# Kernel optimization log

Hardware: AMD Instinct MI355X
Metric: run time of the kernel (lower is better)

## Reference

```python
import jax, jax.numpy as jnp
import numpy as np

B, S, H = 2, 2048, 2048
N_HEADS, N_KV, HEAD_DIM = 16, 8, 128
EPS = 1e-6
ROPE_THETA = 1e6


def _rms_norm(x, w, eps=EPS):
    # per-head RMSNorm over last dim (head_dim), computed in fp32
    xf = x.astype(jnp.float32)
    var = jnp.mean(xf * xf, axis=-1, keepdims=True)
    return (w * (xf * jax.lax.rsqrt(var + eps))).astype(x.dtype)


def _rotate_half(x):
    x1, x2 = jnp.split(x, 2, axis=-1)
    return jnp.concatenate((-x2, x1), axis=-1)


def setup_inputs() -> dict:
    key = jax.random.key(0)
    ks = jax.random.split(key, 6)
    hidden_states = jax.random.normal(ks[0], (B, S, H), dtype=jnp.float32)
    # RoPE tables: [B, S, head_dim]
    inv_freq = 1.0 / (ROPE_THETA ** (np.arange(0, HEAD_DIM, 2, dtype=np.float32) / HEAD_DIM))
    pos = np.arange(S, dtype=np.float32)
    freqs = np.outer(pos, inv_freq)                      # [S, head_dim/2]
    emb = np.concatenate([freqs, freqs], axis=-1)        # [S, head_dim]
    cos = jnp.broadcast_to(jnp.asarray(np.cos(emb)), (B, S, HEAD_DIM))
    sin = jnp.broadcast_to(jnp.asarray(np.sin(emb)), (B, S, HEAD_DIM))
    # additive causal mask [B, 1, S, S]
    causal = jnp.triu(jnp.full((S, S), -1e9, dtype=jnp.float32), k=1)
    attention_mask = jnp.broadcast_to(causal[None, None], (B, 1, S, S))
    scale = 0.02
    Wq = jax.random.normal(ks[1], (N_HEADS * HEAD_DIM, H), dtype=jnp.float32) * scale
    Wk = jax.random.normal(ks[2], (N_KV * HEAD_DIM, H), dtype=jnp.float32) * scale
    Wv = jax.random.normal(ks[3], (N_KV * HEAD_DIM, H), dtype=jnp.float32) * scale
    Wo = jax.random.normal(ks[4], (H, N_HEADS * HEAD_DIM), dtype=jnp.float32) * scale
    q_norm_w = jnp.ones((HEAD_DIM,), dtype=jnp.float32)
    k_norm_w = jnp.ones((HEAD_DIM,), dtype=jnp.float32)
    return dict(hidden_states=hidden_states, cos=cos, sin=sin,
                attention_mask=attention_mask, Wq=Wq, Wk=Wk, Wv=Wv, Wo=Wo,
                q_norm_w=q_norm_w, k_norm_w=k_norm_w)


def reference(hidden_states, cos, sin, attention_mask, Wq, Wk, Wv, Wo, q_norm_w, k_norm_w):
    b, s, _ = hidden_states.shape
    scaling = HEAD_DIM ** -0.5
    n_rep = N_HEADS // N_KV
    # QKV projections (torch Linear: x @ W.T), split into heads
    q = jnp.einsum('bsh,dh->bsd', hidden_states, Wq).reshape(b, s, N_HEADS, HEAD_DIM)
    k = jnp.einsum('bsh,dh->bsd', hidden_states, Wk).reshape(b, s, N_KV, HEAD_DIM)
    v = jnp.einsum('bsh,dh->bsd', hidden_states, Wv).reshape(b, s, N_KV, HEAD_DIM)
    # per-head QK RMSNorm, then [B, H, S, D]
    q = _rms_norm(q, q_norm_w).transpose(0, 2, 1, 3)
    k = _rms_norm(k, k_norm_w).transpose(0, 2, 1, 3)
    v = v.transpose(0, 2, 1, 3)
    # RoPE (cos/sin unsqueezed over head dim)
    c = cos[:, None, :, :]
    sn = sin[:, None, :, :]
    q = q * c + _rotate_half(q) * sn
    k = k * c + _rotate_half(k) * sn
    # GQA: repeat kv heads
    k = jnp.repeat(k, n_rep, axis=1)
    v = jnp.repeat(v, n_rep, axis=1)
    # eager attention: materialize full [B, H, S, S] scores
    attn_weights = jnp.einsum('bhqd,bhkd->bhqk', q, k) * scaling + attention_mask
    attn_weights = jax.nn.softmax(attn_weights.astype(jnp.float32), axis=-1).astype(q.dtype)
    attn_output = jnp.einsum('bhqk,bhkd->bhqd', attn_weights, v)
    attn_output = attn_output.transpose(0, 2, 1, 3).reshape(b, s, N_HEADS * HEAD_DIM)
    attn_output = jnp.einsum('bsd,hd->bsh', attn_output, Wo)
    return attn_output, attn_weights
```

## Files before the change

### kernel.cpp

```cpp
#include <hip/hip_runtime.h>
#include <stdint.h>

typedef unsigned short u16;
typedef __attribute__((ext_vector_type(8))) short bf16x8;
typedef __attribute__((ext_vector_type(4))) float f32x4;
typedef __attribute__((ext_vector_type(8))) unsigned short u16x8;

#define SCALE_LOG2E 0.12751743007633614f

__device__ __forceinline__ u16 f2bf(float x){
  uint32_t u = __float_as_uint(x);
  u += 0x7FFFu + ((u >> 16) & 1u);
  return (u16)(u >> 16);
}
__device__ __forceinline__ float bf2f(u16 h){
  return __uint_as_float(((uint32_t)h) << 16);
}
__device__ __forceinline__ void gload16(const void* g, void* l){
  __builtin_amdgcn_global_load_lds((const __attribute__((address_space(1))) void*)g,
                                   (__attribute__((address_space(3))) void*)l, 16, 0, 0);
}

__global__ __launch_bounds__(256) void k_cvt5(
    const float* __restrict__ s0, u16* __restrict__ d0,
    const float* __restrict__ s1, u16* __restrict__ d1,
    const float* __restrict__ s2, u16* __restrict__ d2,
    const float* __restrict__ s3, u16* __restrict__ d3,
    const float* __restrict__ s4, u16* __restrict__ d4)
{
  int b = blockIdx.x;
  const float* s; u16* d; int off;
  if      (b < 8192)  { s=s0; d=d0; off=b; }
  else if (b < 12288) { s=s1; d=d1; off=b-8192; }
  else if (b < 14336) { s=s2; d=d2; off=b-12288; }
  else if (b < 16384) { s=s3; d=d3; off=b-14336; }
  else                { s=s4; d=d4; off=b-16384; }
  size_t i = ((size_t)off * 256 + threadIdx.x) * 4;
  float4 v = *(const float4*)(s + i);
  ushort4 o;
  o.x = f2bf(v.x); o.y = f2bf(v.y); o.z = f2bf(v.z); o.w = f2bf(v.w);
  *(ushort4*)(d + i) = o;
}

#define STAGE_UNIT(PTR, ROWOFF, BUF, TENS, KS, T1) do{ \
  _Pragma("unroll") \
  for(int jj=0;jj<2;jj++){ \
    int rs_ = wid*32 + jj*16 + (lane>>2); \
    int kp_ = (lane&3) ^ ((rs_>>1)&3); \
    gload16((PTR) + (size_t)((ROWOFF)+rs_)*K + (size_t)(T1)*64 + (KS)*32 + kp_*8, \
            &lds[BUF][TENS][KS][(wid*2+jj)*512]); \
  }}while(0)

#define FRAG(BASE, ROW) (*(const bf16x8*)((BASE) + (ROW)*32 + ((c_ ^ (((ROW)>>1)&3))<<3)))

__global__ __launch_bounds__(512,2) void k_gemm256(
    const u16* __restrict__ A, const u16* __restrict__ Bw, void* __restrict__ Cout,
    int N, int K, int ldc, int out_f32)
{
  __shared__ u16 lds[2][2][2][256*32];
  const int tid = threadIdx.x, wid = tid>>6, lane = tid&63;
  const int nbn = N >> 8;
  const int cpx = gridDim.x >> 3;
  const int bid = (blockIdx.x & 7)*cpx + (blockIdx.x >> 3);
  const int bm = bid / nbn, bn = bid % nbn;
  const int m0 = bm<<8, n0 = bn<<8;
  const int wm = wid>>2, wn = wid&3;
  const int c_ = lane>>4, rl = lane&15;

  f32x4 acc[8][4];
  f32x4 zero4 = {0.f,0.f,0.f,0.f};
#pragma unroll
  for (int i=0;i<8;i++)
#pragma unroll
    for (int j=0;j<4;j++) acc[i][j] = zero4;

  STAGE_UNIT(A,  m0, 0, 0, 0, 0);
  STAGE_UNIT(Bw, n0, 0, 1, 0, 0);
  STAGE_UNIT(A,  m0, 0, 0, 1, 0);
  STAGE_UNIT(Bw, n0, 0, 1, 1, 0);

  const int nt = K >> 6;
#pragma unroll 2
  for (int t=0; t<nt; ++t) {
    const int cur = t&1, nxt = cur^1;
    const bool pf = (t+1 < nt);
    const u16* Ab0 = lds[cur][0][0];
    const u16* Bb0 = lds[cur][1][0];
    const u16* Ab1 = lds[cur][0][1];
    const u16* Bb1 = lds[cur][1][1];
    bf16x8 af[4], bf[4];

    asm volatile("s_waitcnt vmcnt(4)" ::: "memory");
    __builtin_amdgcn_s_barrier();
    asm volatile("" ::: "memory");
#pragma unroll
    for (int j=0;j<4;j++) bf[j] = FRAG(Bb0, wn*64 + j*16 + rl);
#pragma unroll
    for (int i=0;i<4;i++) af[i] = FRAG(Ab0, wm*128 + i*16 + rl);
    if (pf) STAGE_UNIT(A, m0, nxt, 0, 0, t+1);
    __builtin_amdgcn_s_setprio(1);
#pragma unroll
    for (int i=0;i<4;i++)
#pragma unroll
      for (int j=0;j<4;j++)
        acc[i][j] = __builtin_amdgcn_mfma_f32_16x16x32_bf16(af[i], bf[j], acc[i][j], 0,0,0);
    __builtin_amdgcn_s_setprio(0);
    __builtin_amdgcn_s_barrier();
    asm volatile("" ::: "memory");

#pragma unroll
    for (int i=0;i<4;i++) af[i] = FRAG(Ab0, wm*128 + (i+4)*16 + rl);
    if (pf) STAGE_UNIT(Bw, n0, nxt, 1, 0, t+1);
    __builtin_amdgcn_s_setprio(1);
#pragma unroll
    for (int i=0;i<4;i++)
#pragma unroll
      for (int j=0;j<4;j++)
        acc[i+4][j] = __builtin_amdgcn_mfma_f32_16x16x32_bf16(af[i], bf[j], acc[i+4][j], 0,0,0);
    __builtin_amdgcn_s_setprio(0);
    __builtin_amdgcn_s_barrier();
    asm volatile("" ::: "memory");

    if (pf) { asm volatile("s_waitcnt vmcnt(4)" ::: "memory"); }
    else    { asm volatile("s_waitcnt vmcnt(0)" ::: "memory"); }
    __builtin_amdgcn_s_barrier();
    asm volatile("" ::: "memory");
#pragma unroll
    for (int j=0;j<4;j++) bf[j] = FRAG(Bb1, wn*64 + j*16 + rl);
#pragma unroll
    for (int i=0;i<4;i++) af[i] = FRAG(Ab1, wm*128 + i*16 + rl);
    if (pf) STAGE_UNIT(A, m0, nxt, 0, 1, t+1);
    __builtin_amdgcn_s_setprio(1);
#pragma unroll
    for (int i=0;i<4;i++)
#pragma unroll
      for (int j=0;j<4;j++)
        acc[i][j] = __builtin_amdgcn_mfma_f32_16x16x32_bf16(af[i], bf[j], acc[i][j], 0,0,0);
    __builtin_amdgcn_s_setprio(0);
    __builtin_amdgcn_s_barrier();
    asm volatile("" ::: "memory");

#pragma unroll
    for (int i=0;i<4;i++) af[i] = FRAG(Ab1, wm*128 + (i+4)*16 + rl);
    if (pf) STAGE_UNIT(Bw, n0, nxt, 1, 1, t+1);
    __builtin_amdgcn_s_setprio(1);
#pragma unroll
    for (int i=0;i<4;i++)
#pragma unroll
      for (int j=0;j<4;j++)
        acc[i+4][j] = __builtin_amdgcn_mfma_f32_16x16x32_bf16(af[i], bf[j], acc[i+4][j], 0,0,0);
    __builtin_amdgcn_s_setprio(0);
    __builtin_amdgcn_s_barrier();
    asm volatile("" ::: "memory");
  }

  const int r0 = m0 + wm*128 + ((lane>>4)<<2);
  const int c0 = n0 + wn*64 + rl;
  if (out_f32) {
    float* C = (float*)Cout;
#pragma unroll
    for (int i=0;i<8;i++)
#pragma unroll
      for (int j=0;j<4;j++)
#pragma unroll
        for (int r=0;r<4;r++)
          C[(size_t)(r0 + i*16 + r)*ldc + (c0 + j*16)] = acc[i][j][r];
  } else {
    u16* C = (u16*)Cout;
#pragma unroll
    for (int i=0;i<8;i++)
#pragma unroll
      for (int j=0;j<4;j++)
#pragma unroll
        for (int r=0;r<4;r++)
          C[(size_t)(r0 + i*16 + r)*ldc + (c0 + j*16)] = f2bf(acc[i][j][r]);
  }
}

#define STAGE_A128(BUF, KS, T1) do{ \
  int rs_ = wid*16 + (lane>>2); \
  int kp_ = (lane&3) ^ ((rs_>>1)&3); \
  gload16(A + (size_t)(m0+rs_)*K + (size_t)(T1)*64 + (KS)*32 + kp_*8, \
          &ldsA[BUF][KS][wid*512]); \
  }while(0)

#define STAGE_B128(BUF, KS, T1) do{ \
  _Pragma("unroll") \
  for(int jj=0;jj<2;jj++){ \
    int rs_ = wid*32 + jj*16 + (lane>>2); \
    int kp_ = (lane&3) ^ ((rs_>>1)&3); \
    gload16(Bw + (size_t)(n0+rs_)*K + (size_t)(T1)*64 + (KS)*32 + kp_*8, \
            &ldsB[BUF][KS][(wid*2+jj)*512]); \
  }}while(0)

__global__ __launch_bounds__(512,2) void k_gemm_bm128(
    const u16* __restrict__ A, const u16* __restrict__ Bw, float* __restrict__ C,
    int N, int K, int ldc)
{
  __shared__ u16 ldsA[2][2][128*32];
  __shared__ u16 ldsB[2][2][256*32];
  const int tid = threadIdx.x, wid = tid>>6, lane = tid&63;
  const int nbn = N >> 8;
  const int cpx = gridDim.x >> 3;
  const int bid = (blockIdx.x & 7)*cpx + (blockIdx.x >> 3);
  const int bm = bid / nbn, bn = bid % nbn;
  const int m0 = bm<<7, n0 = bn<<8;
  const int wm = wid>>2, wn = wid&3;
  const int c_ = lane>>4, rl = lane&15;

  f32x4 acc[4][4];
  f32x4 zero4 = {0.f,0.f,0.f,0.f};
#pragma unroll
  for (int i=0;i<4;i++)
#pragma unroll
    for (int j=0;j<4;j++) acc[i][j] = zero4;

  STAGE_A128(0, 0, 0);
  STAGE_B128(0, 0, 0);
  STAGE_A128(0, 1, 0);
  STAGE_B128(0, 1, 0);

  const int nt = K >> 6;
#pragma unroll 2
  for (int t=0; t<nt; ++t) {
    const int cur = t&1, nxt = cur^1;
    const bool pf = (t+1 < nt);
    bf16x8 af[4], bf[4];

    asm volatile("s_waitcnt vmcnt(3)" ::: "memory");
    __builtin_amdgcn_s_barrier();
    asm volatile("" ::: "memory");
#pragma unroll
    for (int i=0;i<4;i++) af[i] = FRAG(ldsA[cur][0], wm*64 + i*16 + rl);
#pragma unroll
    for (int j=0;j<4;j++) bf[j] = FRAG(ldsB[cur][0], wn*64 + j*16 + rl);
    if (pf) { STAGE_A128(nxt, 0, t+1); STAGE_B128(nxt, 0, t+1); }
    __builtin_amdgcn_s_setprio(1);
#pragma unroll
    for (int i=0;i<4;i++)
#pragma unroll
      for (int j=0;j<4;j++)
        acc[i][j] = __builtin_amdgcn_mfma_f32_16x16x32_bf16(af[i], bf[j], acc[i][j], 0,0,0);
    __builtin_amdgcn_s_setprio(0);
    __builtin_amdgcn_s_barrier();
    asm volatile("" ::: "memory");

    if (pf) { asm volatile("s_waitcnt vmcnt(3)" ::: "memory"); }
    else    { asm volatile("s_waitcnt vmcnt(0)" ::: "memory"); }
    __builtin_amdgcn_s_barrier();
    asm volatile("" ::: "memory");
#pragma unroll
    for (int i=0;i<4;i++) af[i] = FRAG(ldsA[cur][1], wm*64 + i*16 + rl);
#pragma unroll
    for (int j=0;j<4;j++) bf[j] = FRAG(ldsB[cur][1], wn*64 + j*16 + rl);
    if (pf) { STAGE_A128(nxt, 1, t+1); STAGE_B128(nxt, 1, t+1); }
    __builtin_amdgcn_s_setprio(1);
#pragma unroll
    for (int i=0;i<4;i++)
#pragma unroll
      for (int j=0;j<4;j++)
        acc[i][j] = __builtin_amdgcn_mfma_f32_16x16x32_bf16(af[i], bf[j], acc[i][j], 0,0,0);
    __builtin_amdgcn_s_setprio(0);
    __builtin_amdgcn_s_barrier();
    asm volatile("" ::: "memory");
  }

  const int r0 = m0 + wm*64 + ((lane>>4)<<2);
  const int c0 = n0 + wn*64 + rl;
#pragma unroll
  for (int i=0;i<4;i++)
#pragma unroll
    for (int j=0;j<4;j++)
#pragma unroll
      for (int r=0;r<4;r++)
        C[(size_t)(r0 + i*16 + r)*ldc + (c0 + j*16)] = acc[i][j][r];
}

__global__ __launch_bounds__(256) void k_normrope(
    u16* __restrict__ qkv, const float* __restrict__ cosb, const float* __restrict__ sinb,
    const float* __restrict__ qw, const float* __restrict__ kw)
{
  const int tid = threadIdx.x, lane = tid&63;
  const int task = blockIdx.x*4 + (tid>>6);
  int bs, col; const float* w;
  if (task < 65536) { bs = task >> 4; col = (task & 15)*128; w = qw; }
  else { int t2 = task - 65536; bs = t2 >> 3; col = 2048 + (t2 & 7)*128; w = kw; }
  u16* row = qkv + (size_t)bs*4096 + col;
  float x0 = bf2f(row[lane]), x1 = bf2f(row[lane+64]);
  float ss = x0*x0 + x1*x1;
#pragma unroll
  for (int m=1; m<64; m<<=1) ss += __shfl_xor(ss, m, 64);
  float rn = rsqrtf(ss*(1.0f/128.0f) + 1e-6f);
  const float* cp = cosb + (size_t)bs*128;
  const float* sp = sinb + (size_t)bs*128;
  float q0 = x0*rn*w[lane], q1 = x1*rn*w[lane+64];
  float o0 = q0*cp[lane]    - q1*sp[lane];
  float o1 = q1*cp[lane+64] + q0*sp[lane+64];
  row[lane]    = f2bf(o0);
  row[lane+64] = f2bf(o1);
}

__global__ __launch_bounds__(256) void k_vtrans(const u16* __restrict__ qkv, u16* __restrict__ vt)
{
  const int bid = blockIdx.x;
  const int dt = bid & 1, st = (bid>>1)&31, kvh = (bid>>6)&7, b = bid>>9;
  __shared__ u16 tile[64][72];
  const int tid = threadIdx.x;
  const int rr = tid >> 3, c = (tid & 7) * 8;
  const u16* src = qkv + ((size_t)(b*2048 + st*64))*4096 + 3072 + kvh*128 + dt*64;
#pragma unroll
  for (int p=0;p<2;p++){
    int sl = p*32 + rr;
    u16x8 v = *(const u16x8*)(src + (size_t)sl*4096 + c);
#pragma unroll
    for (int e=0;e<8;e++) tile[sl][c+e] = v[e];
  }
  __syncthreads();
  u16* dst = vt + ((size_t)((b*8+kvh)*128 + dt*64))*2048 + st*64;
#pragma unroll
  for (int p=0;p<2;p++){
    int dl = p*32 + rr;
    u16x8 o;
#pragma unroll
    for (int e=0;e<8;e++) o[e] = tile[c+e][dl];
    *(u16x8*)(dst + (size_t)dl*2048 + c) = o;
  }
}

#define STAGE_K(T, DSTBUF) do { \
  _Pragma("unroll") \
  for (int i_=0;i_<4;i_++){ \
    int r_ = wv*16 + i_*4 + (lane>>4); \
    int cs_ = (lane&15) ^ (r_&7); \
    gload16(Kb + (size_t)((T)*64 + r_)*4096 + cs_*8, (DSTBUF) + (wv*4+i_)*512); \
  } } while(0)

#define STAGE_V(T, DSTBUF) do { \
  _Pragma("unroll") \
  for (int i_=0;i_<4;i_++){ \
    int d_ = wv*32 + i_*8 + (lane>>3); \
    int cs_ = (lane&7) ^ (d_&7); \
    gload16(Vb + (size_t)d_*2048 + (T)*64 + cs_*8, (DSTBUF) + (wv*4+i_)*512); \
  } } while(0)

#define COMPUTE_S(SACC, KBUF) do { \
  _Pragma("unroll") \
  for (int ks_=0;ks_<4;ks_++){ \
    bf16x8 bfr_[4]; \
    _Pragma("unroll") \
    for (int ns_=0;ns_<4;ns_++){ \
      int n_ = ns_*16 + (lane&15); \
      int sl_ = (ks_*4 + (lane>>4)) ^ (n_&7); \
      bfr_[ns_] = *(const bf16x8*)((KBUF) + n_*128 + sl_*8); \
    } \
    _Pragma("unroll") \
    for (int ms_=0;ms_<2;ms_++) \
      _Pragma("unroll") \
      for (int ns_=0;ns_<4;ns_++) \
        SACC[ms_][ns_] = __builtin_amdgcn_mfma_f32_16x16x32_bf16(qf[ms_][ks_], bfr_[ns_], SACC[ms_][ns_], 0,0,0); \
  } } while(0)

__global__ __launch_bounds__(256) void k_attn(
    const u16* __restrict__ qkv, const u16* __restrict__ vt,
    float* __restrict__ probs, u16* __restrict__ attn_o)
{
  __shared__ u16 lK[2][64*128];
  __shared__ u16 lV[2][128*64];
  __shared__ u16 lP[4][32*64];
  const int tid = threadIdx.x, wv = tid>>6, lane = tid&63;
  const int bid = blockIdx.x;
  const int r9 = bid >> 5;
  const int qt = (r9 < 8) ? (15 - r9) : (r9 - 8);
  const int bh = bid & 31;
  const int h = bh & 15, b = bh >> 4;
  const int kvh = h>>1;
  const int q0 = qt<<7;
  const u16* Qb = qkv + (size_t)b*2048*4096 + h*128;
  const u16* Kb = qkv + (size_t)b*2048*4096 + 2048 + kvh*128;
  const u16* Vb = vt + (size_t)(b*8+kvh)*128*2048;

  f32x4 zero4 = {0.f,0.f,0.f,0.f};

  bf16x8 qf[2][4];
#pragma unroll
  for (int ms=0;ms<2;ms++)
#pragma unroll
    for (int ks=0;ks<4;ks++){
      int r = q0 + wv*32 + ms*16 + (lane&15);
      int cc = ks*32 + (lane>>4)*8;
      qf[ms][ks] = *(const bf16x8*)(Qb + (size_t)r*4096 + cc);
    }

  const int nkt = 2*qt + 2;
  float lsum[2][4];
#pragma unroll
  for (int ms=0;ms<2;ms++)
#pragma unroll
    for (int r=0;r<4;r++) lsum[ms][r] = 0.f;

  int cur = 0;
  STAGE_K(0, lK[0]);
  asm volatile("s_waitcnt vmcnt(0)" ::: "memory");
  __syncthreads();
  for (int t=0; t<nkt; ++t) {
    if (t+1 < nkt) STAGE_K(t+1, lK[cur^1]);
    f32x4 sacc[2][4];
#pragma unroll
    for (int ms=0;ms<2;ms++)
#pragma unroll
      for (int ns=0;ns<4;ns++) sacc[ms][ns] = zero4;
    COMPUTE_S(sacc, lK[cur]);
    const int rb = q0 + wv*32 + ((lane>>4)<<2);
    const int cb = t*64 + (lane&15);
#pragma unroll
    for (int ms=0;ms<2;ms++)
#pragma unroll
      for (int ns=0;ns<4;ns++)
#pragma unroll
        for (int r=0;r<4;r++){
          int rg = rb + ms*16 + r, cg = cb + ns*16;
          float e = __builtin_exp2f(sacc[ms][ns][r]*SCALE_LOG2E);
          lsum[ms][r] += (cg <= rg) ? e : 0.f;
        }
    asm volatile("s_waitcnt vmcnt(0)" ::: "memory");
    __syncthreads();
    cur ^= 1;
  }
#pragma unroll
  for (int m=1;m<16;m<<=1)
#pragma unroll
    for (int ms=0;ms<2;ms++)
#pragma unroll
      for (int r=0;r<4;r++) lsum[ms][r] += __shfl_xor(lsum[ms][r], m, 64);
  float linv[2][4];
#pragma unroll
  for (int ms=0;ms<2;ms++)
#pragma unroll
    for (int r=0;r<4;r++) linv[ms][r] = 1.0f / lsum[ms][r];

  f32x4 oacc[2][8];
#pragma unroll
  for (int ms=0;ms<2;ms++)
#pragma unroll
    for (int nd=0;nd<8;nd++) oacc[ms][nd] = zero4;

  u16* pw = lP[wv];
  float* pb = probs + (size_t)(b*16+h)*2048*2048;

  cur = 0;
  STAGE_K(0, lK[0]);
  STAGE_V(0, lV[0]);
  asm volatile("s_waitcnt vmcnt(0)" ::: "memory");
  __syncthreads();
  for (int t=0; t<nkt; ++t) {
    if (t+1 < nkt) { STAGE_K(t+1, lK[cur^1]); STAGE_V(t+1, lV[cur^1]); }
    asm volatile("" ::: "memory");
    f32x4 sacc[2][4];
#pragma unroll
    for (int ms=0;ms<2;ms++)
#pragma unroll
      for (int ns=0;ns<4;ns++) sacc[ms][ns] = zero4;
    COMPUTE_S(sacc, lK[cur]);
    const int rb = q0 + wv*32 + ((lane>>4)<<2);
    const int cb = t*64 + (lane&15);
#pragma unroll
    for (int ms=0;ms<2;ms++)
#pragma unroll
      for (int ns=0;ns<4;ns++)
#pragma unroll
        for (int r=0;r<4;r++){
          int rg = rb + ms*16 + r, cg = cb + ns*16;
          float p = (cg <= rg) ? __builtin_exp2f(sacc[ms][ns][r]*SCALE_LOG2E)*linv[ms][r] : 0.f;
          __builtin_nontemporal_store(p, pb + (size_t)rg*2048 + cg);
          int ql = ms*16 + ((lane>>4)<<2) + r;
          int kl = ns*16 + (lane&15);
          pw[ql*64 + (((kl>>3) ^ (ql&7))<<3) + (kl&7)] = f2bf(p);
        }
    const u16* vbuf = lV[cur];
#pragma unroll
    for (int kks=0;kks<2;kks++){
      bf16x8 pa[2];
#pragma unroll
      for (int ms=0;ms<2;ms++){
        int ql = ms*16 + (lane&15);
        int sl = (kks*4 + (lane>>4)) ^ (ql&7);
        pa[ms] = *(const bf16x8*)(pw + ql*64 + sl*8);
      }
#pragma unroll
      for (int nd=0;nd<8;nd++){
        int d = nd*16 + (lane&15);
        int sl = (kks*4 + (lane>>4)) ^ (d&7);
        bf16x8 vb = *(const bf16x8*)(vbuf + d*64 + sl*8);
#pragma unroll
        for (int ms=0;ms<2;ms++)
          oacc[ms][nd] = __builtin_amdgcn_mfma_f32_16x16x32_bf16(pa[ms], vb, oacc[ms][nd], 0,0,0);
      }
    }
    if (t+1 < nkt) {
      asm volatile("s_waitcnt vmcnt(32)" ::: "memory");
      __syncthreads();
    }
    cur ^= 1;
  }

  const int kend = nkt*64;
  f32x4 z4 = {0.f,0.f,0.f,0.f};
  for (int q = wv*32; q < wv*32+32; ++q){
    float* rp = pb + (size_t)(q0 + q)*2048;
    for (int c = kend + lane*4; c < 2048; c += 256)
      __builtin_nontemporal_store(z4, (f32x4*)(rp + c));
  }

#pragma unroll
  for (int ms=0;ms<2;ms++)
#pragma unroll
    for (int nd=0;nd<8;nd++)
#pragma unroll
      for (int r=0;r<4;r++){
        int rg = q0 + wv*32 + ms*16 + ((lane>>4)<<2) + r;
        int cg = h*128 + nd*16 + (lane&15);
        attn_o[(size_t)(b*2048 + rg)*2048 + cg] = f2bf(oacc[ms][nd][r]);
      }
}

extern "C" void kernel_launch(void* const* d_in, const int* in_sizes, int n_in,
                              void* d_out, int out_size, void* d_ws, size_t ws_size,
                              hipStream_t stream) {
  (void)in_sizes; (void)n_in; (void)out_size; (void)ws_size;
  const float* hs   = (const float*)d_in[0];
  const float* cosb = (const float*)d_in[1];
  const float* sinb = (const float*)d_in[2];
  const float* Wq   = (const float*)d_in[4];
  const float* Wk   = (const float*)d_in[5];
  const float* Wv   = (const float*)d_in[6];
  const float* Wo   = (const float*)d_in[7];
  const float* qw   = (const float*)d_in[8];
  const float* kw   = (const float*)d_in[9];
  float* out   = (float*)d_out;
  float* probs = out + 8388608;

  char* ws = (char*)d_ws;
  u16* hs_b   = (u16*)(ws);
  u16* attn_o = hs_b;
  u16* W_all  = (u16*)(ws + (16u<<20));
  u16* Wo_b   = (u16*)(ws + (32u<<20));
  u16* qkv    = (u16*)(ws + (40u<<20));
  u16* v_t    = (u16*)(ws + (72u<<20));

  k_cvt5<<<20480,256,0,stream>>>(hs, hs_b, Wq, W_all, Wk, W_all + 4194304,
                                 Wv, W_all + 6291456, Wo, Wo_b);

  k_gemm256<<<256,512,0,stream>>>(hs_b, W_all, (void*)qkv, 4096, 2048, 4096, 0);
  k_normrope<<<24576,256,0,stream>>>(qkv, cosb, sinb, qw, kw);
  k_vtrans<<<1024,256,0,stream>>>(qkv, v_t);
  k_attn<<<512,256,0,stream>>>(qkv, v_t, probs, attn_o);
  k_gemm_bm128<<<256,512,0,stream>>>(attn_o, Wo_b, out, 2048, 2048, 2048);
}
```

Baseline: 376.0 us.

## Deepen K prefetch, skip masked tiles per wave, vectorize probability stores

Reworks the attention kernel in several ways. The pass that computes row sums now uses a 4-buffer K ring with prefetch three tiles ahead. Each wave skips score tiles past its own causal diagonal, and the mask test is applied only on the diagonal tile. In the output pass, probabilities are read back from the bf16 LDS tile and written as 16-byte float4 nontemporal stores instead of scalar stores. The trailing zero-fill then starts at each wave's diagonal. The stored fp32 probabilities now hold bf16-rounded values, which loses some precision, and waitcnt counts are hand-tuned.

```diff
diff --git a/kernel.cpp b/kernel.cpp
--- a/kernel.cpp
+++ b/kernel.cpp
@@ -4,6 +4,7 @@
 typedef unsigned short u16;
 typedef __attribute__((ext_vector_type(8))) short bf16x8;
 typedef __attribute__((ext_vector_type(4))) float f32x4;
+typedef __attribute__((ext_vector_type(4))) unsigned short u16x4;
 typedef __attribute__((ext_vector_type(8))) unsigned short u16x8;
 
 #define SCALE_LOG2E 0.12751743007633614f
@@ -364,8 +365,7 @@
     const u16* __restrict__ qkv, const u16* __restrict__ vt,
     float* __restrict__ probs, u16* __restrict__ attn_o)
 {
-  __shared__ u16 lK[2][64*128];
-  __shared__ u16 lV[2][128*64];
+  __shared__ u16 lKV[4][64*128];
   __shared__ u16 lP[4][32*64];
   const int tid = threadIdx.x, wv = tid>>6, lane = tid&63;
   const int bid = blockIdx.x;
@@ -392,118 +392,148 @@
     }
 
   const int nkt = 2*qt + 2;
+  const int tdiag = 2*qt + (wv>>1);
   float lsum[2][4];
 #pragma unroll
   for (int ms=0;ms<2;ms++)
 #pragma unroll
     for (int r=0;r<4;r++) lsum[ms][r] = 0.f;
 
+  STAGE_K(0, lKV[0]);
+  STAGE_K(1, lKV[1]);
+  if (nkt > 2) STAGE_K(2, lKV[2]);
+  for (int t=0; t<nkt; ++t) {
+    if      (t+2 < nkt) { asm volatile("s_waitcnt vmcnt(8)" ::: "memory"); }
+    else if (t+1 < nkt) { asm volatile("s_waitcnt vmcnt(4)" ::: "memory"); }
+    else                { asm volatile("s_waitcnt vmcnt(0)" ::: "memory"); }
+    __syncthreads();
+    if (t+3 < nkt) STAGE_K(t+3, lKV[(t+3)&3]);
+    asm volatile("" ::: "memory");
+    if (t <= tdiag) {
+      f32x4 sacc[2][4];
+#pragma unroll
+      for (int ms=0;ms<2;ms++)
+#pragma unroll
+        for (int ns=0;ns<4;ns++) sacc[ms][ns] = zero4;
+      COMPUTE_S(sacc, lKV[t&3]);
+      const int rb = q0 + wv*32 + ((lane>>4)<<2);
+      const int cb = t*64 + (lane&15);
+      if (t == tdiag) {
+#pragma unroll
+        for (int ms=0;ms<2;ms++)
+#pragma unroll
+          for (int ns=0;ns<4;ns++)
+#pragma unroll
+            for (int r=0;r<4;r++){
+              int rg = rb + ms*16 + r, cg = cb + ns*16;
+              float e = __builtin_exp2f(sacc[ms][ns][r]*SCALE_LOG2E);
+              lsum[ms][r] += (cg <= rg) ? e : 0.f;
+            }
+      } else {
+#pragma unroll
+        for (int ms=0;ms<2;ms++)
+#pragma unroll
+          for (int ns=0;ns<4;ns++)
+#pragma unroll
+            for (int r=0;r<4;r++)
+              lsum[ms][r] += __builtin_exp2f(sacc[ms][ns][r]*SCALE_LOG2E);
+      }
+    }
+  }
+#pragma unroll
+  for (int m=1;m<16;m<<=1)
+#pragma unroll
+    for (int ms=0;ms<2;ms++)
+#pragma unroll
+      for (int r=0;r<4;r++) lsum[ms][r] += __shfl_xor(lsum[ms][r], m, 64);
+  float linv[2][4];
+#pragma unroll
+  for (int ms=0;ms<2;ms++)
+#pragma unroll
+    for (int r=0;r<4;r++) linv[ms][r] = 1.0f / lsum[ms][r];
+
+  f32x4 oacc[2][8];
+#pragma unroll
+  for (int ms=0;ms<2;ms++)
+#pragma unroll
+    for (int nd=0;nd<8;nd++) oacc[ms][nd] = zero4;
+
+  u16* pw = lP[wv];
+  float* pb = probs + (size_t)(b*16+h)*2048*2048;
+
   int cur = 0;
-  STAGE_K(0, lK[0]);
+  STAGE_K(0, lKV[0]);
+  STAGE_V(0, lKV[2]);
   asm volatile("s_waitcnt vmcnt(0)" ::: "memory");
   __syncthreads();
   for (int t=0; t<nkt; ++t) {
-    if (t+1 < nkt) STAGE_K(t+1, lK[cur^1]);
-    f32x4 sacc[2][4];
-#pragma unroll
-    for (int ms=0;ms<2;ms++)
-#pragma unroll
-      for (int ns=0;ns<4;ns++) sacc[ms][ns] = zero4;
-    COMPUTE_S(sacc, lK[cur]);
-    const int rb = q0 + wv*32 + ((lane>>4)<<2);
-    const int cb = t*64 + (lane&15);
-#pragma unroll
-    for (int ms=0;ms<2;ms++)
-#pragma unroll
-      for (int ns=0;ns<4;ns++)
-#pragma unroll
-        for (int r=0;r<4;r++){
-          int rg = rb + ms*16 + r, cg = cb + ns*16;
-          float e = __builtin_exp2f(sacc[ms][ns][r]*SCALE_LOG2E);
-          lsum[ms][r] += (cg <= rg) ? e : 0.f;
+    const bool pf = (t+1 < nkt);
+    if (pf) { STAGE_K(t+1, lKV[cur^1]); STAGE_V(t+1, lKV[2+(cur^1)]); }
+    asm volatile("" ::: "memory");
+    if (t <= tdiag) {
+      f32x4 sacc[2][4];
+#pragma unroll
+      for (int ms=0;ms<2;ms++)
+#pragma unroll
+        for (int ns=0;ns<4;ns++) sacc[ms][ns] = zero4;
+      COMPUTE_S(sacc, lKV[cur]);
+      const int rb = q0 + wv*32 + ((lane>>4)<<2);
+      const int cb = t*64 + (lane&15);
+#pragma unroll
+      for (int ms=0;ms<2;ms++)
+#pragma unroll
+        for (int ns=0;ns<4;ns++)
+#pragma unroll
+          for (int r=0;r<4;r++){
+            int rg = rb + ms*16 + r, cg = cb + ns*16;
+            float p = (cg <= rg) ? __builtin_exp2f(sacc[ms][ns][r]*SCALE_LOG2E)*linv[ms][r] : 0.f;
+            int ql = ms*16 + ((lane>>4)<<2) + r;
+            int kl = ns*16 + (lane&15);
+            pw[ql*64 + (((kl>>3) ^ (ql&7))<<3) + (kl&7)] = f2bf(p);
+          }
+      {
+        const int cq = lane&15, grp = cq>>1, off = (cq&1)*4;
+#pragma unroll
+        for (int it=0; it<8; ++it){
+          int row = it*4 + (lane>>4);
+          int slot = grp ^ (row&7);
+          u16x4 pk4 = *(const u16x4*)(pw + row*64 + slot*8 + off);
+          f32x4 pf4;
+#pragma unroll
+          for (int r=0;r<4;r++) pf4[r] = bf2f(pk4[r]);
+          __builtin_nontemporal_store(pf4,
+            (f32x4*)(pb + (size_t)(q0 + wv*32 + row)*2048 + t*64 + cq*4));
         }
-    asm volatile("s_waitcnt vmcnt(0)" ::: "memory");
-    __syncthreads();
-    cur ^= 1;
-  }
-#pragma unroll
-  for (int m=1;m<16;m<<=1)
-#pragma unroll
-    for (int ms=0;ms<2;ms++)
-#pragma unroll
-      for (int r=0;r<4;r++) lsum[ms][r] += __shfl_xor(lsum[ms][r], m, 64);
-  float linv[2][4];
-#pragma unroll
-  for (int ms=0;ms<2;ms++)
-#pragma unroll
-    for (int r=0;r<4;r++) linv[ms][r] = 1.0f / lsum[ms][r];
-
-  f32x4 oacc[2][8];
-#pragma unroll
-  for (int ms=0;ms<2;ms++)
-#pragma unroll
-    for (int nd=0;nd<8;nd++) oacc[ms][nd] = zero4;
-
-  u16* pw = lP[wv];
-  float* pb = probs + (size_t)(b*16+h)*2048*2048;
-
-  cur = 0;
-  STAGE_K(0, lK[0]);
-  STAGE_V(0, lV[0]);
-  asm volatile("s_waitcnt vmcnt(0)" ::: "memory");
-  __syncthreads();
-  for (int t=0; t<nkt; ++t) {
-    if (t+1 < nkt) { STAGE_K(t+1, lK[cur^1]); STAGE_V(t+1, lV[cur^1]); }
-    asm volatile("" ::: "memory");
-    f32x4 sacc[2][4];
-#pragma unroll
-    for (int ms=0;ms<2;ms++)
-#pragma unroll
-      for (int ns=0;ns<4;ns++) sacc[ms][ns] = zero4;
-    COMPUTE_S(sacc, lK[cur]);
-    const int rb = q0 + wv*32 + ((lane>>4)<<2);
-    const int cb = t*64 + (lane&15);
-#pragma unroll
-    for (int ms=0;ms<2;ms++)
-#pragma unroll
-      for (int ns=0;ns<4;ns++)
-#pragma unroll
-        for (int r=0;r<4;r++){
-          int rg = rb + ms*16 + r, cg = cb + ns*16;
-          float p = (cg <= rg) ? __builtin_exp2f(sacc[ms][ns][r]*SCALE_LOG2E)*linv[ms][r] : 0.f;
-          __builtin_nontemporal_store(p, pb + (size_t)rg*2048 + cg);
-          int ql = ms*16 + ((lane>>4)<<2) + r;
-          int kl = ns*16 + (lane&15);
-          pw[ql*64 + (((kl>>3) ^ (ql&7))<<3) + (kl&7)] = f2bf(p);
+      }
+      const u16* vbuf = lKV[2+cur];
+#pragma unroll
+      for (int kks=0;kks<2;kks++){
+        bf16x8 pa[2];
+#pragma unroll
+        for (int ms=0;ms<2;ms++){
+          int ql = ms*16 + (lane&15);
+          int sl = (kks*4 + (lane>>4)) ^ (ql&7);
+          pa[ms] = *(const bf16x8*)(pw + ql*64 + sl*8);
         }
-    const u16* vbuf = lV[cur];
-#pragma unroll
-    for (int kks=0;kks<2;kks++){
-      bf16x8 pa[2];
-#pragma unroll
-      for (int ms=0;ms<2;ms++){
-        int ql = ms*16 + (lane&15);
-        int sl = (kks*4 + (lane>>4)) ^ (ql&7);
-        pa[ms] = *(const bf16x8*)(pw + ql*64 + sl*8);
-      }
-#pragma unroll
-      for (int nd=0;nd<8;nd++){
-        int d = nd*16 + (lane&15);
-        int sl = (kks*4 + (lane>>4)) ^ (d&7);
-        bf16x8 vb = *(const bf16x8*)(vbuf + d*64 + sl*8);
-#pragma unroll
-        for (int ms=0;ms<2;ms++)
-          oacc[ms][nd] = __builtin_amdgcn_mfma_f32_16x16x32_bf16(pa[ms], vb, oacc[ms][nd], 0,0,0);
+#pragma unroll
+        for (int nd=0;nd<8;nd++){
+          int d = nd*16 + (lane&15);
+          int sl = (kks*4 + (lane>>4)) ^ (d&7);
+          bf16x8 vb = *(const bf16x8*)(vbuf + d*64 + sl*8);
+#pragma unroll
+          for (int ms=0;ms<2;ms++)
+            oacc[ms][nd] = __builtin_amdgcn_mfma_f32_16x16x32_bf16(pa[ms], vb, oacc[ms][nd], 0,0,0);
+        }
       }
     }
-    if (t+1 < nkt) {
-      asm volatile("s_waitcnt vmcnt(32)" ::: "memory");
+    if (pf) {
+      asm volatile("s_waitcnt vmcnt(8)" ::: "memory");
       __syncthreads();
     }
     cur ^= 1;
   }
 
-  const int kend = nkt*64;
+  const int kend = (tdiag+1)*64;
   f32x4 z4 = {0.f,0.f,0.f,0.f};
   for (int q = wv*32; q < wv*32+32; ++q){
     float* rp = pb + (size_t)(q0 + q)*2048;
```

Measured after the change: 358.9 us. 1.05x faster.

## Split softmax row-sum into separate tile-parallel kernel and shrink attention q-tile

Applied to the files above, without the earlier changes.

Moves the first pass (softmax denominators) into its own kernel. That kernel spreads the causal lower-triangle 64x64 tiles evenly across blocks and accumulates row sums with atomics. The main attention kernel now uses 64-row q tiles, giving 1024 blocks, and reads the precomputed sums. It writes probabilities as coalesced float4 stores from the bf16 LDS tile instead of scattered scalar stores. This trades extra Q/K reloads, atomics and a memset for better load balance, higher occupancy and better store coalescing. The stored probabilities are now bf16-rounded values.

```diff
diff --git a/kernel.cpp b/kernel.cpp
--- a/kernel.cpp
+++ b/kernel.cpp
@@ -4,6 +4,7 @@
 typedef unsigned short u16;
 typedef __attribute__((ext_vector_type(8))) short bf16x8;
 typedef __attribute__((ext_vector_type(4))) float f32x4;
+typedef __attribute__((ext_vector_type(4))) unsigned short u16x4;
 typedef __attribute__((ext_vector_type(8))) unsigned short u16x8;
 
 #define SCALE_LOG2E 0.12751743007633614f
@@ -343,7 +344,7 @@
     gload16(Vb + (size_t)d_*2048 + (T)*64 + cs_*8, (DSTBUF) + (wv*4+i_)*512); \
   } } while(0)
 
-#define COMPUTE_S(SACC, KBUF) do { \
+#define COMPUTE_S16(SACC, KBUF) do { \
   _Pragma("unroll") \
   for (int ks_=0;ks_<4;ks_++){ \
     bf16x8 bfr_[4]; \
@@ -354,173 +355,214 @@
       bfr_[ns_] = *(const bf16x8*)((KBUF) + n_*128 + sl_*8); \
     } \
     _Pragma("unroll") \
-    for (int ms_=0;ms_<2;ms_++) \
-      _Pragma("unroll") \
-      for (int ns_=0;ns_<4;ns_++) \
-        SACC[ms_][ns_] = __builtin_amdgcn_mfma_f32_16x16x32_bf16(qf[ms_][ks_], bfr_[ns_], SACC[ms_][ns_], 0,0,0); \
+    for (int ns_=0;ns_<4;ns_++) \
+      SACC[ns_] = __builtin_amdgcn_mfma_f32_16x16x32_bf16(qf[ks_], bfr_[ns_], SACC[ns_], 0,0,0); \
   } } while(0)
 
-__global__ __launch_bounds__(256) void k_attn(
+__global__ __launch_bounds__(256) void k_lsum(
+    const u16* __restrict__ qkv, float* __restrict__ lsum)
+{
+  __shared__ u16 lK[2][64*128];
+  const int tid = threadIdx.x, wv = tid>>6, lane = tid&63;
+  const int rl = lane&15, hi = lane>>4;
+  const int bh = blockIdx.x & 31;
+  const int h = bh & 15, b = bh >> 4;
+  const int seg = blockIdx.x >> 5;
+  const int kvh = h>>1;
+  const u16* Qb = qkv + (size_t)b*2048*4096 + h*128;
+  const u16* Kb = qkv + (size_t)b*2048*4096 + 2048 + kvh*128;
+  float* lrow = lsum + (size_t)bh*2048;
+
+  f32x4 zero4 = {0.f,0.f,0.f,0.f};
+  int jj[8], kk[8];
+#pragma unroll
+  for (int i=0;i<8;i++){
+    int t = seg*8 + i;
+    int j = (int)((sqrtf(8.0f*t + 1.0f) - 1.0f)*0.5f);
+    while ((j+1)*(j+2)/2 <= t) j++;
+    while (j*(j+1)/2 > t) j--;
+    jj[i] = j; kk[i] = t - j*(j+1)/2;
+  }
+
+  STAGE_K(kk[0], lK[0]);
+  asm volatile("s_waitcnt vmcnt(0)" ::: "memory");
+  __builtin_amdgcn_s_barrier();
+  asm volatile("" ::: "memory");
+#pragma unroll
+  for (int i=0;i<8;i++){
+    const int j = jj[i], kt = kk[i];
+    if (i+1 < 8) STAGE_K(kk[i+1], lK[(i+1)&1]);
+    asm volatile("" ::: "memory");
+    bf16x8 qf[4];
+#pragma unroll
+    for (int ks=0;ks<4;ks++)
+      qf[ks] = *(const bf16x8*)(Qb + (size_t)(j*64 + wv*16 + rl)*4096 + ks*32 + hi*8);
+    f32x4 sacc[4];
+#pragma unroll
+    for (int ns=0;ns<4;ns++) sacc[ns] = zero4;
+    COMPUTE_S16(sacc, lK[i&1]);
+    const int rb = j*64 + wv*16 + hi*4;
+    float part[4] = {0.f,0.f,0.f,0.f};
+    if (kt == j) {
+#pragma unroll
+      for (int ns=0;ns<4;ns++)
+#pragma unroll
+        for (int r=0;r<4;r++){
+          int rg = rb + r, cg = kt*64 + ns*16 + rl;
+          float e = __builtin_exp2f(sacc[ns][r]*SCALE_LOG2E);
+          part[r] += (cg <= rg) ? e : 0.f;
+        }
+    } else {
+#pragma unroll
+      for (int ns=0;ns<4;ns++)
+#pragma unroll
+        for (int r=0;r<4;r++)
+          part[r] += __builtin_exp2f(sacc[ns][r]*SCALE_LOG2E);
+    }
+#pragma unroll
+    for (int m=1;m<16;m<<=1)
+#pragma unroll
+      for (int r=0;r<4;r++) part[r] += __shfl_xor(part[r], m, 64);
+    if (rl == 0) {
+#pragma unroll
+      for (int r=0;r<4;r++) atomicAdd(&lrow[rb + r], part[r]);
+    }
+    if (i+1 < 8) {
+      asm volatile("s_waitcnt vmcnt(4)" ::: "memory");
+      __builtin_amdgcn_s_barrier();
+      asm volatile("" ::: "memory");
+    }
+  }
+}
+
+__global__ __launch_bounds__(256) void k_attn2(
     const u16* __restrict__ qkv, const u16* __restrict__ vt,
-    float* __restrict__ probs, u16* __restrict__ attn_o)
+    const float* __restrict__ lsum, float* __restrict__ probs, u16* __restrict__ attn_o)
 {
   __shared__ u16 lK[2][64*128];
   __shared__ u16 lV[2][128*64];
-  __shared__ u16 lP[4][32*64];
+  __shared__ u16 lP[4][16*64];
   const int tid = threadIdx.x, wv = tid>>6, lane = tid&63;
-  const int bid = blockIdx.x;
-  const int r9 = bid >> 5;
-  const int qt = (r9 < 8) ? (15 - r9) : (r9 - 8);
-  const int bh = bid & 31;
+  const int rl = lane&15, hi = lane>>4;
+  const int j = 31 - (blockIdx.x >> 5);
+  const int bh = blockIdx.x & 31;
   const int h = bh & 15, b = bh >> 4;
   const int kvh = h>>1;
-  const int q0 = qt<<7;
+  const int q0 = j<<6;
   const u16* Qb = qkv + (size_t)b*2048*4096 + h*128;
   const u16* Kb = qkv + (size_t)b*2048*4096 + 2048 + kvh*128;
   const u16* Vb = vt + (size_t)(b*8+kvh)*128*2048;
 
   f32x4 zero4 = {0.f,0.f,0.f,0.f};
 
-  bf16x8 qf[2][4];
-#pragma unroll
-  for (int ms=0;ms<2;ms++)
-#pragma unroll
-    for (int ks=0;ks<4;ks++){
-      int r = q0 + wv*32 + ms*16 + (lane&15);
-      int cc = ks*32 + (lane>>4)*8;
-      qf[ms][ks] = *(const bf16x8*)(Qb + (size_t)r*4096 + cc);
-    }
-
-  const int nkt = 2*qt + 2;
-  float lsum[2][4];
-#pragma unroll
-  for (int ms=0;ms<2;ms++)
-#pragma unroll
-    for (int r=0;r<4;r++) lsum[ms][r] = 0.f;
+  bf16x8 qf[4];
+#pragma unroll
+  for (int ks=0;ks<4;ks++)
+    qf[ks] = *(const bf16x8*)(Qb + (size_t)(q0 + wv*16 + rl)*4096 + ks*32 + hi*8);
+
+  const int nkt = j + 1;
+  const int rb = q0 + wv*16 + hi*4;
+  float linv[4];
+#pragma unroll
+  for (int r=0;r<4;r++) linv[r] = 1.0f / lsum[(size_t)bh*2048 + rb + r];
+
+  f32x4 oacc[8];
+#pragma unroll
+  for (int nd=0;nd<8;nd++) oacc[nd] = zero4;
+
+  u16* pw = lP[wv];
+  float* pb = probs + (size_t)bh*2048*2048;
 
   int cur = 0;
-  STAGE_K(0, lK[0]);
-  asm volatile("s_waitcnt vmcnt(0)" ::: "memory");
-  __syncthreads();
-  for (int t=0; t<nkt; ++t) {
-    if (t+1 < nkt) STAGE_K(t+1, lK[cur^1]);
-    f32x4 sacc[2][4];
-#pragma unroll
-    for (int ms=0;ms<2;ms++)
-#pragma unroll
-      for (int ns=0;ns<4;ns++) sacc[ms][ns] = zero4;
-    COMPUTE_S(sacc, lK[cur]);
-    const int rb = q0 + wv*32 + ((lane>>4)<<2);
-    const int cb = t*64 + (lane&15);
-#pragma unroll
-    for (int ms=0;ms<2;ms++)
-#pragma unroll
-      for (int ns=0;ns<4;ns++)
-#pragma unroll
-        for (int r=0;r<4;r++){
-          int rg = rb + ms*16 + r, cg = cb + ns*16;
-          float e = __builtin_exp2f(sacc[ms][ns][r]*SCALE_LOG2E);
-          lsum[ms][r] += (cg <= rg) ? e : 0.f;
-        }
-    asm volatile("s_waitcnt vmcnt(0)" ::: "memory");
-    __syncthreads();
-    cur ^= 1;
-  }
-#pragma unroll
-  for (int m=1;m<16;m<<=1)
-#pragma unroll
-    for (int ms=0;ms<2;ms++)
-#pragma unroll
-      for (int r=0;r<4;r++) lsum[ms][r] += __shfl_xor(lsum[ms][r], m, 64);
-  float linv[2][4];
-#pragma unroll
-  for (int ms=0;ms<2;ms++)
-#pragma unroll
-    for (int r=0;r<4;r++) linv[ms][r] = 1.0f / lsum[ms][r];
-
-  f32x4 oacc[2][8];
-#pragma unroll
-  for (int ms=0;ms<2;ms++)
-#pragma unroll
-    for (int nd=0;nd<8;nd++) oacc[ms][nd] = zero4;
-
-  u16* pw = lP[wv];
-  float* pb = probs + (size_t)(b*16+h)*2048*2048;
-
-  cur = 0;
   STAGE_K(0, lK[0]);
   STAGE_V(0, lV[0]);
   asm volatile("s_waitcnt vmcnt(0)" ::: "memory");
-  __syncthreads();
+  __builtin_amdgcn_s_barrier();
+  asm volatile("" ::: "memory");
   for (int t=0; t<nkt; ++t) {
-    if (t+1 < nkt) { STAGE_K(t+1, lK[cur^1]); STAGE_V(t+1, lV[cur^1]); }
-    asm volatile("" ::: "memory");
-    f32x4 sacc[2][4];
-#pragma unroll
-    for (int ms=0;ms<2;ms++)
-#pragma unroll
-      for (int ns=0;ns<4;ns++) sacc[ms][ns] = zero4;
-    COMPUTE_S(sacc, lK[cur]);
-    const int rb = q0 + wv*32 + ((lane>>4)<<2);
-    const int cb = t*64 + (lane&15);
-#pragma unroll
-    for (int ms=0;ms<2;ms++)
+    const bool pf = (t+1 < nkt);
+    if (pf) { STAGE_K(t+1, lK[cur^1]); STAGE_V(t+1, lV[cur^1]); }
+    asm volatile("" ::: "memory");
+    f32x4 sacc[4];
+#pragma unroll
+    for (int ns=0;ns<4;ns++) sacc[ns] = zero4;
+    COMPUTE_S16(sacc, lK[cur]);
+    const int cb = t*64;
+    if (t == nkt-1) {
 #pragma unroll
       for (int ns=0;ns<4;ns++)
 #pragma unroll
         for (int r=0;r<4;r++){
-          int rg = rb + ms*16 + r, cg = cb + ns*16;
-          float p = (cg <= rg) ? __builtin_exp2f(sacc[ms][ns][r]*SCALE_LOG2E)*linv[ms][r] : 0.f;
-          __builtin_nontemporal_store(p, pb + (size_t)rg*2048 + cg);
-          int ql = ms*16 + ((lane>>4)<<2) + r;
-          int kl = ns*16 + (lane&15);
+          int rg = rb + r, cg = cb + ns*16 + rl;
+          float p = (cg <= rg) ? __builtin_exp2f(sacc[ns][r]*SCALE_LOG2E)*linv[r] : 0.f;
+          int ql = hi*4 + r, kl = ns*16 + rl;
           pw[ql*64 + (((kl>>3) ^ (ql&7))<<3) + (kl&7)] = f2bf(p);
         }
+    } else {
+#pragma unroll
+      for (int ns=0;ns<4;ns++)
+#pragma unroll
+        for (int r=0;r<4;r++){
+          float p = __builtin_exp2f(sacc[ns][r]*SCALE_LOG2E)*linv[r];
+          int ql = hi*4 + r, kl = ns*16 + rl;
+          pw[ql*64 + (((kl>>3) ^ (ql&7))<<3) + (kl&7)] = f2bf(p);
+        }
+    }
+    {
+      const int cq = rl, grp = cq>>1, off = (cq&1)*4;
+#pragma unroll
+      for (int it=0; it<4; ++it){
+        int row = it*4 + hi;
+        int slot = grp ^ (row&7);
+        u16x4 pk4 = *(const u16x4*)(pw + row*64 + slot*8 + off);
+        f32x4 pf4;
+#pragma unroll
+        for (int r=0;r<4;r++) pf4[r] = bf2f(pk4[r]);
+        __builtin_nontemporal_store(pf4,
+          (f32x4*)(pb + (size_t)(q0 + wv*16 + row)*2048 + t*64 + cq*4));
+      }
+    }
     const u16* vbuf = lV[cur];
 #pragma unroll
     for (int kks=0;kks<2;kks++){
-      bf16x8 pa[2];
-#pragma unroll
-      for (int ms=0;ms<2;ms++){
-        int ql = ms*16 + (lane&15);
-        int sl = (kks*4 + (lane>>4)) ^ (ql&7);
-        pa[ms] = *(const bf16x8*)(pw + ql*64 + sl*8);
+      bf16x8 pa;
+      {
+        int ql = rl;
+        int sl = (kks*4 + hi) ^ (ql&7);
+        pa = *(const bf16x8*)(pw + ql*64 + sl*8);
       }
 #pragma unroll
       for (int nd=0;nd<8;nd++){
-        int d = nd*16 + (lane&15);
-        int sl = (kks*4 + (lane>>4)) ^ (d&7);
+        int d = nd*16 + rl;
+        int sl = (kks*4 + hi) ^ (d&7);
         bf16x8 vb = *(const bf16x8*)(vbuf + d*64 + sl*8);
-#pragma unroll
-        for (int ms=0;ms<2;ms++)
-          oacc[ms][nd] = __builtin_amdgcn_mfma_f32_16x16x32_bf16(pa[ms], vb, oacc[ms][nd], 0,0,0);
+        oacc[nd] = __builtin_amdgcn_mfma_f32_16x16x32_bf16(pa, vb, oacc[nd], 0,0,0);
       }
     }
-    if (t+1 < nkt) {
-      asm volatile("s_waitcnt vmcnt(32)" ::: "memory");
-      __syncthreads();
+    if (pf) {
+      asm volatile("s_waitcnt vmcnt(4)" ::: "memory");
+      __builtin_amdgcn_s_barrier();
+      asm volatile("" ::: "memory");
     }
     cur ^= 1;
   }
 
   const int kend = nkt*64;
   f32x4 z4 = {0.f,0.f,0.f,0.f};
-  for (int q = wv*32; q < wv*32+32; ++q){
+  for (int q = wv*16; q < wv*16+16; ++q){
     float* rp = pb + (size_t)(q0 + q)*2048;
     for (int c = kend + lane*4; c < 2048; c += 256)
       __builtin_nontemporal_store(z4, (f32x4*)(rp + c));
   }
 
 #pragma unroll
-  for (int ms=0;ms<2;ms++)
-#pragma unroll
-    for (int nd=0;nd<8;nd++)
-#pragma unroll
-      for (int r=0;r<4;r++){
-        int rg = q0 + wv*32 + ms*16 + ((lane>>4)<<2) + r;
-        int cg = h*128 + nd*16 + (lane&15);
-        attn_o[(size_t)(b*2048 + rg)*2048 + cg] = f2bf(oacc[ms][nd][r]);
-      }
+  for (int nd=0;nd<8;nd++)
+#pragma unroll
+    for (int r=0;r<4;r++){
+      int rg = rb + r;
+      int cg = h*128 + nd*16 + rl;
+      attn_o[(size_t)(b*2048 + rg)*2048 + cg] = f2bf(oacc[nd][r]);
+    }
 }
 
 extern "C" void kernel_launch(void* const* d_in, const int* in_sizes, int n_in,
@@ -546,13 +588,16 @@
   u16* Wo_b   = (u16*)(ws + (32u<<20));
   u16* qkv    = (u16*)(ws + (40u<<20));
   u16* v_t    = (u16*)(ws + (72u<<20));
-
+  float* lsum = (float*)(ws + (80u<<20));
+
+  hipMemsetAsync(lsum, 0, 65536*sizeof(float), stream);
   k_cvt5<<<20480,256,0,stream>>>(hs, hs_b, Wq, W_all, Wk, W_all + 4194304,
                                  Wv, W_all + 6291456, Wo, Wo_b);
 
   k_gemm256<<<256,512,0,stream>>>(hs_b, W_all, (void*)qkv, 4096, 2048, 4096, 0);
   k_normrope<<<24576,256,0,stream>>>(qkv, cosb, sinb, qw, kw);
+  k_lsum<<<2112,256,0,stream>>>(qkv, lsum);
   k_vtrans<<<1024,256,0,stream>>>(qkv, v_t);
-  k_attn<<<512,256,0,stream>>>(qkv, v_t, probs, attn_o);
+  k_attn2<<<1024,256,0,stream>>>(qkv, v_t, lsum, probs, attn_o);
   k_gemm_bm128<<<256,512,0,stream>>>(attn_o, Wo_b, out, 2048, 2048, 2048);
 }
```

Result: faster. 368.4 us (-2.0%).
